# Kernel optimization log

Measured on AMD Instinct MI355X. Metric: run time of the kernel, lower is better.

Reference implementation:

```python
import jax, jax.numpy as jnp
import numpy as np

B, NQ, C = 4, 3136, 512
H_IMG, W_IMG = 56, 56
HEADS, D_MODEL, D_K, D_V = 8, 512, 512, 512
RATIO = 2
LN_EPS = 1e-3   # keras LayerNormalization default
BN_EPS = 1e-3   # keras BatchNormalization default


def setup_inputs() -> dict:
    key = jax.random.key(0)
    ks = jax.random.split(key, 16)
    s = 0.02
    inp = {
        'queries': jax.random.normal(ks[0], (B, NQ, C), jnp.float32),
        'keys': jax.random.normal(ks[1], (B, NQ, C), jnp.float32),
        'values': jax.random.normal(ks[2], (B, NQ, C), jnp.float32),
        'Wq': jax.random.normal(ks[3], (C, HEADS * D_K), jnp.float32) * s,
        'bq': jnp.zeros((HEADS * D_K,), jnp.float32),
        'Wk': jax.random.normal(ks[4], (C, HEADS * D_K), jnp.float32) * s,
        'bk': jnp.zeros((HEADS * D_K,), jnp.float32),
        'Wv': jax.random.normal(ks[5], (C, HEADS * D_V), jnp.float32) * s,
        'bv': jnp.zeros((HEADS * D_V,), jnp.float32),
        'Wo': jax.random.normal(ks[6], (HEADS * D_V, D_MODEL), jnp.float32) * s,
        'bo': jnp.zeros((D_MODEL,), jnp.float32),
        # depthwise conv: kernel (kh, kw, in_per_group=1, out=C)
        'sr_kernel': jax.random.normal(ks[7], (RATIO + 1, RATIO + 1, 1, C), jnp.float32) * s,
        'sr_bias': jnp.zeros((C,), jnp.float32),
        'ln_gamma': jnp.ones((C,), jnp.float32),
        'ln_beta': jnp.zeros((C,), jnp.float32),
        # 1x1 channels_first conv over the head axis of the score tensor
        'tw': jax.random.normal(ks[8], (HEADS, HEADS), jnp.float32) * s,
        'tb': jnp.zeros((HEADS,), jnp.float32),
        # BatchNormalization(axis=[0,1]) -> params per (batch, head)
        'bn_gamma': jnp.ones((B, HEADS), jnp.float32),
        'bn_beta': jnp.zeros((B, HEADS), jnp.float32),
    }
    return inp


def _forward(queries, keys, values, Wq, bq, Wk, bk, Wv, bv, Wo, bo,
             sr_kernel, sr_bias, ln_gamma, ln_beta, tw, tb, bn_gamma, bn_beta):
    b, nq, c = queries.shape
    # Q projection -> (b, h, nq, d_model)  (d_k == d_model)
    q = (queries @ Wq + bq).reshape(b, nq, HEADS, D_MODEL).transpose(0, 2, 1, 3)
    # spatial reduction of K/V source (ratio > 1 path; keys/values args unused)
    x = queries.reshape(b, H_IMG, W_IMG, c)
    x = jax.lax.conv_general_dilated(
        x, sr_kernel, window_strides=(RATIO, RATIO), padding='SAME',
        dimension_numbers=('NHWC', 'HWIO', 'NHWC'), feature_group_count=c) + sr_bias
    x = x.reshape(b, -1, c)  # (b, nk, c), nk = (H/ratio)*(W/ratio)
    mu = jnp.mean(x, axis=-1, keepdims=True)
    var = jnp.mean(jnp.square(x - mu), axis=-1, keepdims=True)
    x = (x - mu) * jax.lax.rsqrt(var + LN_EPS) * ln_gamma + ln_beta
    k = (x @ Wk + bk).reshape(b, -1, HEADS, D_MODEL).transpose(0, 2, 1, 3)
    v = (x @ Wv + bv).reshape(b, -1, HEADS, D_MODEL).transpose(0, 2, 1, 3)
    # scores (b, h, nq, nk)
    att = jnp.einsum('bhqd,bhkd->bhqk', q, k) / np.sqrt(D_K).astype(np.float32)
    # transform: 1x1 conv over head channel, softmax over k, BN over (q, k)
    att = jnp.einsum('bhqk,hg->bgqk', att, tw) + tb[:, None, None]
    att = jax.nn.softmax(att, axis=-1)
    m = jnp.mean(att, axis=(2, 3), keepdims=True)
    s2 = jnp.mean(jnp.square(att - m), axis=(2, 3), keepdims=True)
    att = bn_gamma[:, :, None, None] * (att - m) * jax.lax.rsqrt(s2 + BN_EPS) \
          + bn_beta[:, :, None, None]
    # attend and project out
    out = jnp.einsum('bhqk,bhkd->bhqd', att, v)
    out = out.transpose(0, 2, 1, 3).reshape(b, nq, HEADS * D_V)
    return out @ Wo + bo


def reference(queries, keys, values, Wq, bq, Wk, bk, Wv, bv, Wo, bo,
              sr_kernel, sr_bias, ln_gamma, ln_beta, tw, tb, bn_gamma, bn_beta):
    return _forward(queries, keys, values, Wq, bq, Wk, bk, Wv, bv, Wo, bo,
                    sr_kernel, sr_bias, ln_gamma, ln_beta, tw, tb, bn_gamma, bn_beta)
```

## Files before the change

### kernel.cpp

```cpp
#include <hip/hip_runtime.h>
#include <hip/hip_bf16.h>
#include <math.h>

typedef unsigned short u16;
typedef __attribute__((ext_vector_type(4))) float f32x4;
typedef __attribute__((ext_vector_type(8))) __bf16 bf16x8;

#define B_    4
#define NQ_   3136
#define C_    512
#define HIMG  56
#define WIMG  56
#define HD_   4096
#define NK_   784
#define NKP_  832

static __device__ __forceinline__ float b2f(u16 u){
  union { unsigned int i; float f; } v; v.i = ((unsigned int)u)<<16; return v.f;
}
static __device__ __forceinline__ u16 f2b(float f){
  union { float f; unsigned int i; } v; v.f = f;
  unsigned int r = v.i + 0x7fffu + ((v.i>>16)&1u);
  return (u16)(r>>16);
}

#define GLD16(gsrc, ldst) __builtin_amdgcn_global_load_lds( \
    (const __attribute__((address_space(1))) void*)(gsrc), \
    (__attribute__((address_space(3))) void*)(ldst), 16, 0, 0)

static __device__ __forceinline__ void xcd_swz(int &bx, int &by, int &bz){
  const long nx = gridDim.x, ny = gridDim.y, nz = gridDim.z;
  const long l = blockIdx.x + nx*(blockIdx.y + ny*(long)blockIdx.z);
  const long n = nx*ny*nz;
  const long q8 = n>>3, r8 = n&7;
  const long xcd = l&7, idx = l>>3;
  const long wg = (xcd<r8 ? xcd*(q8+1) : r8*(q8+1) + (xcd-r8)*q8) + idx;
  by = (int)(wg % ny);
  bx = (int)((wg/ny) % nx);
  bz = (int)(wg/(nx*ny));
}

__global__ __launch_bounds__(512)
void gemm256(const u16* __restrict__ A, const u16* __restrict__ Bm, u16* __restrict__ Cm,
             int M, int Ncols, int K, int sA, int sB, int sC, int zdiv,
             long long zA1, long long zA2, long long zB1, long long zB2,
             long long zC1, long long zC2,
             const float* __restrict__ bias1, float hscale,
             const float* __restrict__ scalePtr)
{
  __shared__ u16 lds[73728];
  int bx, by, z;
  xcd_swz(bx, by, z);
  const int zq = z / zdiv, zr = z % zdiv;
  const u16* Ab = A  + (long long)zq*zA1 + (long long)zr*zA2;
  const u16* Bb = Bm + (long long)zq*zB1 + (long long)zr*zB2;
  const int m0 = bx*256, n0 = by*128;
  const int t = threadIdx.x, w = t>>6, lane = t&63;
  const int wm = w>>1, wn = w&1;
  const int l15 = lane & 15;

  const int srow = t>>3;
  const int scol = (((t&7) ^ ((t>>3)&7)) << 3);
  const u16* aS = Ab + (long long)(m0 + srow)*sA + scol;
  const u16* bS = Bb + (long long)(n0 + srow)*sB + scol;
  const long long sA64 = (long long)64*sA, sB64 = (long long)64*sB;
  const int w512 = w*512;

#define STAGE_H0(jt, buf) do{                                     \
    const u16* a0_ = aS + (long long)(jt)*64;                     \
    u16* la_ = lds + (buf)*16384 + w512;                          \
    GLD16(a0_,            la_);                                   \
    GLD16(a0_ +   sA64,   la_ + 4096);                            \
    GLD16(a0_ + 2*sA64,   la_ + 8192);                            \
  }while(0)
#define STAGE_H1(jt, buf) do{                                     \
    const u16* a0_ = aS + (long long)(jt)*64;                     \
    const u16* b0_ = bS + (long long)(jt)*64;                     \
    u16* la_ = lds + (buf)*16384 + w512;                          \
    u16* lb_ = lds + 49152 + (buf)*8192 + w512;                   \
    GLD16(a0_ + 3*sA64,   la_ + 12288);                           \
    GLD16(b0_,            lb_);                                   \
    GLD16(b0_ +   sB64,   lb_ + 4096);                            \
  }while(0)

  f32x4 acc[4][4];
#pragma unroll
  for(int i=0;i<4;i++)
#pragma unroll
    for(int j=0;j<4;j++) acc[i][j] = (f32x4)(0.0f);

  const char* ldsc = (const char*)lds;
  const int ck0 = (((lane>>4)     ^ (lane&7)) << 4);
  const int ck1 = (((4+(lane>>4)) ^ (lane&7)) << 4);
  const int aRowB = (wm*64 + l15) * 128;
  const int bRowB = (wn*64 + l15) * 128;

  const int T = K >> 6;
  STAGE_H0(0, 0); STAGE_H1(0, 0);
  STAGE_H0(1, 1); STAGE_H1(1, 1);

  int buf = 0;
  for(int j=0; j<T; j++){
    if(j == T-1) asm volatile("s_waitcnt vmcnt(0)" ::: "memory");
    else         asm volatile("s_waitcnt vmcnt(6)" ::: "memory");
    asm volatile("s_barrier" ::: "memory");

    const int aBuf = buf*32768 + aRowB;
    const int bBuf = 98304 + buf*16384 + bRowB;
    const int nbuf = (buf+2 >= 3) ? buf-1 : buf+2;
    {
      bf16x8 af[4], bf[4];
#pragma unroll
      for(int fr=0; fr<4; fr++) af[fr] = *(const bf16x8*)(ldsc + aBuf + fr*2048 + ck0);
#pragma unroll
      for(int fn=0; fn<4; fn++) bf[fn] = *(const bf16x8*)(ldsc + bBuf + fn*2048 + ck0);
      if(j+2 < T) STAGE_H0(j+2, nbuf);
      asm volatile("s_barrier" ::: "memory");
      __builtin_amdgcn_s_setprio(1);
#pragma unroll
      for(int fr=0; fr<4; fr++)
#pragma unroll
        for(int fn=0; fn<4; fn++)
          acc[fr][fn] = __builtin_amdgcn_mfma_f32_16x16x32_bf16(af[fr], bf[fn], acc[fr][fn], 0,0,0);
      __builtin_amdgcn_s_setprio(0);
    }
    {
      bf16x8 af[4], bf[4];
#pragma unroll
      for(int fr=0; fr<4; fr++) af[fr] = *(const bf16x8*)(ldsc + aBuf + fr*2048 + ck1);
#pragma unroll
      for(int fn=0; fn<4; fn++) bf[fn] = *(const bf16x8*)(ldsc + bBuf + fn*2048 + ck1);
      if(j+2 < T) STAGE_H1(j+2, nbuf);
      asm volatile("s_barrier" ::: "memory");
      __builtin_amdgcn_s_setprio(1);
#pragma unroll
      for(int fr=0; fr<4; fr++)
#pragma unroll
        for(int fn=0; fn<4; fn++)
          acc[fr][fn] = __builtin_amdgcn_mfma_f32_16x16x32_bf16(af[fr], bf[fn], acc[fr][fn], 0,0,0);
      __builtin_amdgcn_s_setprio(0);
    }
    buf = (buf+1 >= 3) ? 0 : buf+1;
  }
#undef STAGE_H0
#undef STAGE_H1

  const float dsc = scalePtr ? scalePtr[z] : 1.0f;
  const long long cBase = (long long)zq*zC1 + (long long)zr*zC2;
  const int r4 = (lane>>4)*4;
#pragma unroll
  for(int mf=0; mf<4; mf++){
    const int row0 = m0 + wm*64 + mf*16 + r4;
#pragma unroll
    for(int nf=0; nf<4; nf++){
      const int col = n0 + wn*64 + nf*16 + l15;
      if(col < Ncols){
#pragma unroll
        for(int r=0;r<4;r++){
          const int row = row0 + r;
          if(row < M){
            float v = acc[mf][nf][r];
            if(bias1) v += bias1[col];
            Cm[cBase + (long long)row*sC + col] = f2b(v * hscale * dsc);
          }
        }
      }
    }
  }
}

template<int OUT_F32>
__global__ __launch_bounds__(256)
void gemm_bt(const u16* __restrict__ A, const u16* __restrict__ Bm, void* __restrict__ Cm,
             int M, int K, int sA, int sB, int sC, int zdiv,
             long long zA1, long long zA2, long long zB1, long long zB2,
             long long zC1, long long zC2,
             const float* __restrict__ bias1, float hscale,
             const float* __restrict__ scalePtr,
             const float* __restrict__ bias2, int rowsPerB, int b2s)
{
  __shared__ u16 lA[128*32];
  __shared__ u16 lB[128*32];
  int bx, by, z;
  xcd_swz(bx, by, z);
  const int zq = z / zdiv, zr = z % zdiv;
  const u16* Ab = A  + (long long)zq*zA1 + (long long)zr*zA2;
  const u16* Bb = Bm + (long long)zq*zB1 + (long long)zr*zB2;
  const int m0 = bx*128, n0 = by*128;
  const int t = threadIdx.x, wave = t>>6, lane = t&63;
  const int wm = (wave>>1)*64, wn = (wave&1)*64;
  const int lrow = t>>2, lcol = (t&3)*8;

  const u16* aSrc = Ab + (long long)(m0+lrow)*sA + lcol;
  const u16* bSrc = Bb + (long long)(n0+lrow)*sB + lcol;
  u16* lAw = lA + wave*512;
  u16* lBw = lB + wave*512;

  f32x4 acc[4][4];
#pragma unroll
  for(int i=0;i<4;i++)
#pragma unroll
    for(int j=0;j<4;j++) acc[i][j] = (f32x4)(0.0f);

  const int l16 = lane & 15, lk8 = (lane>>4)*8;

  for(int kk=0; kk<K; kk+=32){
    GLD16(aSrc,                    lAw);
    GLD16(aSrc + (long long)64*sA, lAw + 64*32);
    GLD16(bSrc,                    lBw);
    GLD16(bSrc + (long long)64*sB, lBw + 64*32);
    aSrc += 32; bSrc += 32;
    __syncthreads();
    bf16x8 af[4], bfr[4];
#pragma unroll
    for(int i=0;i<4;i++){
      af[i]  = *(const bf16x8*)(lA + (wm + i*16 + l16)*32 + lk8);
      bfr[i] = *(const bf16x8*)(lB + (wn + i*16 + l16)*32 + lk8);
    }
#pragma unroll
    for(int i=0;i<4;i++)
#pragma unroll
      for(int j=0;j<4;j++)
        acc[i][j] = __builtin_amdgcn_mfma_f32_16x16x32_bf16(af[i], bfr[j], acc[i][j], 0,0,0);
    __syncthreads();
  }

  const float dsc = scalePtr ? scalePtr[z] : 1.0f;
  const long long cBase = (long long)zq*zC1 + (long long)zr*zC2;
  const int rbase = (lane>>4)*4;
#pragma unroll
  for(int i=0;i<4;i++){
#pragma unroll
    for(int j=0;j<4;j++){
#pragma unroll
      for(int r=0;r<4;r++){
        const int row = m0 + wm + i*16 + rbase + r;
        const int col = n0 + wn + j*16 + l16;
        if(row < M){
          float v = acc[i][j][r];
          if(bias1) v += bias1[col];
          v *= hscale * dsc;
          if(bias2) v += bias2[(row/rowsPerB)*b2s + col];
          if(OUT_F32) ((float*)Cm)[cBase + (long long)row*sC + col] = v;
          else        ((u16*) Cm)[cBase + (long long)row*sC + col] = f2b(v);
        }
      }
    }
  }
}

__global__ __launch_bounds__(256)
void wt_kernel(const float* __restrict__ W, u16* __restrict__ Wt, int K, int N){
  __shared__ float tile[32][33];
  const int n0 = blockIdx.x*32, k0 = blockIdx.y*32;
  const int t = threadIdx.x, tr = t>>5, tc = t&31;
#pragma unroll
  for(int i=0;i<4;i++)
    tile[tr+i*8][tc] = W[(long long)(k0+tr+i*8)*N + n0+tc];
  __syncthreads();
#pragma unroll
  for(int i=0;i<4;i++)
    Wt[(long long)(n0+tr+i*8)*K + k0+tc] = f2b(tile[tc][tr+i*8]);
}

__global__ __launch_bounds__(256)
void cvt_bf16(const float* __restrict__ in, u16* __restrict__ outp, long long n){
  long long i = ((long long)blockIdx.x*256 + threadIdx.x)*4;
  if(i+3 < n){
    float4 v = *(const float4*)(in+i);
    ushort4 o; o.x=f2b(v.x); o.y=f2b(v.y); o.z=f2b(v.z); o.w=f2b(v.w);
    *(ushort4*)(outp+i) = o;
  }
}

__global__ __launch_bounds__(256)
void conv_ln(const float* __restrict__ q, const float* __restrict__ ker,
             const float* __restrict__ cbias, const float* __restrict__ gamma,
             const float* __restrict__ beta, u16* __restrict__ xo)
{
  const int p = blockIdx.x;
  const int b = p / 784, pix = p % 784;
  const int oy = pix / 28, ox = pix % 28;
  const int t = threadIdx.x;
  __shared__ float red[256];
  float v[2];
#pragma unroll
  for(int e=0;e<2;e++){
    const int c = t + e*256;
    float acc = cbias[c];
    for(int ky=0;ky<3;ky++){
      const int y = oy*2 + ky;
      if(y >= HIMG) continue;
      for(int kx=0;kx<3;kx++){
        const int x = ox*2 + kx;
        if(x >= WIMG) continue;
        acc += q[(((long long)b*HIMG + y)*WIMG + x)*C_ + c] * ker[(ky*3+kx)*C_ + c];
      }
    }
    v[e] = acc;
  }
  red[t]=v[0]+v[1]; __syncthreads();
  for(int st=128; st>0; st>>=1){ if(t<st) red[t]+=red[t+st]; __syncthreads(); }
  const float mu = red[0] * (1.0f/C_);
  __syncthreads();
  const float d0=v[0]-mu, d1=v[1]-mu;
  red[t]=d0*d0+d1*d1; __syncthreads();
  for(int st=128; st>0; st>>=1){ if(t<st) red[t]+=red[t+st]; __syncthreads(); }
  const float rs = rsqrtf(red[0]*(1.0f/C_) + 1e-3f);
  const long long ob = (long long)p*C_;
#pragma unroll
  for(int e=0;e<2;e++){
    const int c = t+e*256;
    xo[ob+c] = f2b((v[e]-mu)*rs*gamma[c] + beta[c]);
  }
}

__global__ __launch_bounds__(256)
void vt_kernel(const u16* __restrict__ Vf_b, u16* __restrict__ Vt_b, int sV){
  __shared__ u16 tile[32][33];
  const int k0 = blockIdx.x*32, d0 = blockIdx.y*32;
  const int t = threadIdx.x, tr = t>>5, tc = t&31;
#pragma unroll
  for(int i=0;i<4;i++){
    const int k = k0+tr+i*8;
    tile[tr+i*8][tc] = (k < NK_) ? Vf_b[(long long)k*sV + d0+tc] : (u16)0;
  }
  __syncthreads();
#pragma unroll
  for(int i=0;i<4;i++)
    Vt_b[(long long)(d0+tr+i*8)*NKP_ + k0+tc] = tile[tc][tr+i*8];
}

__global__ __launch_bounds__(512)
void mix_softmax(u16* __restrict__ S_b, const float* __restrict__ tw,
                 float* __restrict__ partial_b)
{
  const int qi = blockIdx.x;
  const int t = threadIdx.x;
  const int wave = t >> 6, lane = t & 63;
  __shared__ float sv[8*NK_];
  const long long rowstr = (long long)NQ_*NKP_;
  const long long base = (long long)qi*NKP_;

  for(int idx = t; idx < 8*196; idx += 512){
    const int h = idx / 196, c4 = idx % 196;
    ushort4 u4 = *(const ushort4*)(S_b + base + h*rowstr + c4*4);
    float* d = sv + h*NK_ + c4*4;
    d[0]=b2f(u4.x); d[1]=b2f(u4.y); d[2]=b2f(u4.z); d[3]=b2f(u4.w);
  }
  __syncthreads();

  const int g = wave;
  float wgt[8];
#pragma unroll
  for(int h=0;h<8;h++) wgt[h] = tw[h*8+g];

  float xs[13];
  float lmax = -1e30f;
#pragma unroll
  for(int j=0;j<13;j++){
    const int k = j*64 + lane;
    if(k < NK_){
      float x = 0.f;
#pragma unroll
      for(int h=0;h<8;h++) x += wgt[h]*sv[h*NK_+k];
      xs[j] = x;
      lmax = fmaxf(lmax, x);
    } else xs[j] = -1e30f;
  }
#pragma unroll
  for(int off=32; off>=1; off>>=1) lmax = fmaxf(lmax, __shfl_xor(lmax, off));

  float lsum = 0.f;
#pragma unroll
  for(int j=0;j<13;j++){
    const int k = j*64 + lane;
    if(k < NK_){
      const float e = __expf(xs[j] - lmax);
      xs[j] = e; lsum += e;
    }
  }
#pragma unroll
  for(int off=32; off>=1; off>>=1) lsum += __shfl_xor(lsum, off);
  const float inv = 1.0f/lsum;

  u16* dst = S_b + base + g*rowstr;
  float lss = 0.f;
#pragma unroll
  for(int j=0;j<13;j++){
    const int k = j*64 + lane;
    if(k < NK_){
      const float dev = xs[j]*inv - (1.0f/NK_);
      dst[k] = f2b(dev);
      lss += dev*dev;
    }
  }
  for(int k = NK_ + lane; k < NKP_; k += 64) dst[k] = 0;
#pragma unroll
  for(int off=32; off>=1; off>>=1) lss += __shfl_xor(lss, off);
  if(lane==0) partial_b[g*NQ_ + qi] = lss;
}

__global__ __launch_bounds__(256)
void colsum_v(const u16* __restrict__ Vf_b, float* __restrict__ cs_b, int sV){
  const int hd = blockIdx.x*256 + threadIdx.x;
  const u16* p = Vf_b + hd;
  float s=0.f;
  for(int k=0;k<NK_;k++) s += b2f(p[(long long)k*sV]);
  cs_b[hd]=s;
}

__global__ __launch_bounds__(256)
void finalize_stats(const float* __restrict__ partial_b, const float* __restrict__ bng_b,
                    const float* __restrict__ bnb_b, float* __restrict__ a_b,
                    float* __restrict__ c_b){
  const int g = blockIdx.x;
  const int t = threadIdx.x;
  __shared__ float red[4];
  float s = 0.f;
  for(int i=t; i<NQ_; i+=256) s += partial_b[g*NQ_ + i];
#pragma unroll
  for(int off=32; off>=1; off>>=1) s += __shfl_xor(s, off);
  if((t&63)==0) red[t>>6] = s;
  __syncthreads();
  if(t==0){
    const float tot = red[0]+red[1]+red[2]+red[3];
    const float s2 = tot * (1.0f/((float)NQ_*(float)NK_));
    a_b[g] = bng_b[g]*rsqrtf(s2 + 1e-3f);
    c_b[g] = bnb_b[g];
  }
}

__global__ __launch_bounds__(256)
void corr_kernel(const float* __restrict__ cs_b, const u16* __restrict__ Wot,
                 const float* __restrict__ c_b, float* __restrict__ corr_b){
  const int n = blockIdx.x, t = threadIdx.x;
  __shared__ float red[256];
  float s = 0.f;
  for(int hd=t; hd<HD_; hd+=256)
    s += c_b[hd>>9] * cs_b[hd] * b2f(Wot[(long long)n*HD_+hd]);
  red[t]=s; __syncthreads();
  for(int st=128; st>0; st>>=1){ if(t<st) red[t]+=red[t+st]; __syncthreads(); }
  if(t==0) corr_b[n]=red[0];
}

extern "C" void kernel_launch(void* const* d_in, const int* in_sizes, int n_in,
                              void* d_out, int out_size, void* d_ws, size_t ws_size,
                              hipStream_t stream)
{
  (void)in_sizes; (void)n_in; (void)out_size;
  const float* queries = (const float*)d_in[0];
  const float* Wq  = (const float*)d_in[3];
  const float* bq  = (const float*)d_in[4];
  const float* Wk  = (const float*)d_in[5];
  const float* bk  = (const float*)d_in[6];
  const float* Wv  = (const float*)d_in[7];
  const float* bv  = (const float*)d_in[8];
  const float* Wo  = (const float*)d_in[9];
  const float* bo  = (const float*)d_in[10];
  const float* srk = (const float*)d_in[11];
  const float* srb = (const float*)d_in[12];
  const float* lng = (const float*)d_in[13];
  const float* lnb = (const float*)d_in[14];
  const float* tw  = (const float*)d_in[15];
  const float* bng = (const float*)d_in[17];
  const float* bnb = (const float*)d_in[18];
  float* out = (float*)d_out;
  const float QSC = 0.04419417382415922f;

  char* w = (char*)d_ws;
  size_t off = 0;
  auto alloc = [&](size_t bytes)->char*{
    char* p = w + off; off += (bytes + 255) & ~(size_t)255; return p;
  };

  const bool tierA = (ws_size >= (size_t)210*1024*1024);

  u16* Wqt = (u16*)alloc((size_t)HD_*C_*2);
  u16* Wkt = (u16*)alloc((size_t)HD_*C_*2);
  u16* Wvt = (u16*)alloc((size_t)HD_*C_*2);
  u16* Wot = (u16*)alloc((size_t)C_*HD_*2);
  u16* x   = (u16*)alloc((size_t)B_*NK_*C_*2 + 262144);
  float* bkv = (float*)alloc((size_t)2*HD_*4);
  u16* Qin;
  u16* QfU;
  if(tierA){
    Qin = (u16*)alloc((size_t)B_*NQ_*C_*2);
    QfU = (u16*)alloc((size_t)B_*NQ_*HD_*2);
  } else {
    Qin = (u16*)alloc((size_t)NQ_*C_*2 + 262144);
    QfU = (u16*)alloc((size_t)NQ_*HD_*2);
  }
  u16* KV_b = (u16*)alloc((size_t)NK_*2*HD_*2 + 4194304);
  u16* Vt_b = (u16*)alloc((size_t)HD_*NKP_*2);
  u16* S_b  = (u16*)alloc((size_t)8*NQ_*NKP_*2 + 524288);
  float* colsum  = (float*)alloc((size_t)B_*HD_*4);
  float* partial = (float*)alloc((size_t)8*NQ_*4);
  float* aArr    = (float*)alloc(256);
  float* cArr    = (float*)alloc(256);
  float* corrB   = (float*)alloc((size_t)B_*C_*4);

  wt_kernel<<<dim3(128,16), 256, 0, stream>>>(Wq, Wqt, 512, 4096);
  wt_kernel<<<dim3(128,16), 256, 0, stream>>>(Wk, Wkt, 512, 4096);
  wt_kernel<<<dim3(128,16), 256, 0, stream>>>(Wv, Wvt, 512, 4096);
  wt_kernel<<<dim3(16,128), 256, 0, stream>>>(Wo, Wot, 4096, 512);
  conv_ln<<<B_*NK_, 256, 0, stream>>>(queries, srk, srb, lng, lnb, x);
  hipMemcpyAsync(bkv,      bk, HD_*4, hipMemcpyDeviceToDevice, stream);
  hipMemcpyAsync(bkv+HD_,  bv, HD_*4, hipMemcpyDeviceToDevice, stream);

  if(tierA){
    cvt_bf16<<<6272, 256, 0, stream>>>(queries, Qin, (long long)B_*NQ_*C_);
    gemm256<<<dim3(49,32,1),512,0,stream>>>(Qin, Wqt, QfU, B_*NQ_, 4096, 512,
        512, 512, HD_, 1, 0,0,0,0,0,0, bq, QSC, nullptr);
  }

  for(int b=0; b<B_; b++){
    u16* Qf_b = tierA ? (QfU + (size_t)b*NQ_*HD_) : QfU;
    if(!tierA){
      cvt_bf16<<<1568, 256, 0, stream>>>(queries + (size_t)b*NQ_*C_, Qin, (long long)NQ_*C_);
      gemm256<<<dim3(13,32,1),512,0,stream>>>(Qin, Wqt, Qf_b, NQ_, 4096, 512,
          512, 512, HD_, 1, 0,0,0,0,0,0, bq, QSC, nullptr);
    }
    const u16* x_b = x + (size_t)b*NK_*C_;
    gemm256<<<dim3(4,64,1),512,0,stream>>>(x_b, Wkt, KV_b, NK_, 2*HD_, 512,
        512, 512, 2*HD_, 1, 0,0,0,0,0,0, bkv, 1.0f, nullptr);
    vt_kernel<<<dim3(26,128),256,0,stream>>>(KV_b + HD_, Vt_b, 2*HD_);
    colsum_v<<<16,256,0,stream>>>(KV_b + HD_, colsum + b*HD_, 2*HD_);
    gemm256<<<dim3(13,7,8),512,0,stream>>>(Qf_b, KV_b, S_b, NQ_, NKP_, 512,
        HD_, 2*HD_, NKP_, 8, 0, 512, 0, 512, 0, (long long)NQ_*NKP_,
        nullptr, 1.0f, nullptr);
    mix_softmax<<<NQ_, 512, 0, stream>>>(S_b, tw, partial);
    finalize_stats<<<8,256,0,stream>>>(partial, bng + b*8, bnb + b*8, aArr + b*8, cArr + b*8);
    corr_kernel<<<512,256,0,stream>>>(colsum + b*HD_, Wot, cArr + b*8, corrB + b*C_);
    gemm256<<<dim3(13,4,8),512,0,stream>>>(S_b, Vt_b, Qf_b, NQ_, 512, NKP_,
        NKP_, NKP_, HD_, 8, 0, (long long)NQ_*NKP_, 0, (long long)512*NKP_, 0, 512,
        nullptr, 1.0f, aArr + b*8);
    if(!tierA){
      gemm_bt<1><<<dim3(25,4,1),256,0,stream>>>(Qf_b, Wot, out + (size_t)b*NQ_*C_,
          NQ_, HD_, HD_, HD_, C_,
          1, 0,0,0,0,0,0, bo, 1.0f, nullptr, corrB + b*C_, NQ_, C_);
    }
  }

  if(tierA){
    gemm_bt<1><<<dim3(98,4,1),256,0,stream>>>(QfU, Wot, out, B_*NQ_, HD_, HD_, HD_, C_,
        1, 0,0,0,0,0,0, bo, 1.0f, nullptr, corrB, NQ_, C_);
  }
}
```

Measured before the change: 1.013 ms.

## Replace 256x128 and simple GEMMs with unified double-buffered 128x128 kernel

Removes the 512-thread 256x128 triple-buffered GEMM and the simple single-buffered gemm_bt. Both are replaced by one templated 128x128-tile, 256-thread kernel with K-step 64, XOR-swizzled LDS, and a double buffer filled by async global-to-LDS loads. All GEMM launches, including the output projection, now use this kernel with grids adjusted for the smaller tiles. This gives more blocks and lower LDS use per block, and a pipelined output projection. In exchange, each block reuses less data per tile and the prefetch pipeline is shallower than the old triple buffer.

```diff
diff --git a/kernel.cpp b/kernel.cpp
--- a/kernel.cpp
+++ b/kernel.cpp
@@ -40,161 +40,48 @@
   bz = (int)(wg/(nx*ny));
 }
 
-__global__ __launch_bounds__(512)
-void gemm256(const u16* __restrict__ A, const u16* __restrict__ Bm, u16* __restrict__ Cm,
+template<int OUT_F32>
+__global__ __launch_bounds__(256)
+void gemm128(const u16* __restrict__ A, const u16* __restrict__ Bm, void* __restrict__ Cm,
              int M, int Ncols, int K, int sA, int sB, int sC, int zdiv,
-             long long zA1, long long zA2, long long zB1, long long zB2,
-             long long zC1, long long zC2,
-             const float* __restrict__ bias1, float hscale,
-             const float* __restrict__ scalePtr)
-{
-  __shared__ u16 lds[73728];
-  int bx, by, z;
-  xcd_swz(bx, by, z);
-  const int zq = z / zdiv, zr = z % zdiv;
-  const u16* Ab = A  + (long long)zq*zA1 + (long long)zr*zA2;
-  const u16* Bb = Bm + (long long)zq*zB1 + (long long)zr*zB2;
-  const int m0 = bx*256, n0 = by*128;
-  const int t = threadIdx.x, w = t>>6, lane = t&63;
-  const int wm = w>>1, wn = w&1;
-  const int l15 = lane & 15;
-
-  const int srow = t>>3;
-  const int scol = (((t&7) ^ ((t>>3)&7)) << 3);
-  const u16* aS = Ab + (long long)(m0 + srow)*sA + scol;
-  const u16* bS = Bb + (long long)(n0 + srow)*sB + scol;
-  const long long sA64 = (long long)64*sA, sB64 = (long long)64*sB;
-  const int w512 = w*512;
-
-#define STAGE_H0(jt, buf) do{                                     \
-    const u16* a0_ = aS + (long long)(jt)*64;                     \
-    u16* la_ = lds + (buf)*16384 + w512;                          \
-    GLD16(a0_,            la_);                                   \
-    GLD16(a0_ +   sA64,   la_ + 4096);                            \
-    GLD16(a0_ + 2*sA64,   la_ + 8192);                            \
-  }while(0)
-#define STAGE_H1(jt, buf) do{                                     \
-    const u16* a0_ = aS + (long long)(jt)*64;                     \
-    const u16* b0_ = bS + (long long)(jt)*64;                     \
-    u16* la_ = lds + (buf)*16384 + w512;                          \
-    u16* lb_ = lds + 49152 + (buf)*8192 + w512;                   \
-    GLD16(a0_ + 3*sA64,   la_ + 12288);                           \
-    GLD16(b0_,            lb_);                                   \
-    GLD16(b0_ +   sB64,   lb_ + 4096);                            \
-  }while(0)
-
-  f32x4 acc[4][4];
-#pragma unroll
-  for(int i=0;i<4;i++)
-#pragma unroll
-    for(int j=0;j<4;j++) acc[i][j] = (f32x4)(0.0f);
-
-  const char* ldsc = (const char*)lds;
-  const int ck0 = (((lane>>4)     ^ (lane&7)) << 4);
-  const int ck1 = (((4+(lane>>4)) ^ (lane&7)) << 4);
-  const int aRowB = (wm*64 + l15) * 128;
-  const int bRowB = (wn*64 + l15) * 128;
-
-  const int T = K >> 6;
-  STAGE_H0(0, 0); STAGE_H1(0, 0);
-  STAGE_H0(1, 1); STAGE_H1(1, 1);
-
-  int buf = 0;
-  for(int j=0; j<T; j++){
-    if(j == T-1) asm volatile("s_waitcnt vmcnt(0)" ::: "memory");
-    else         asm volatile("s_waitcnt vmcnt(6)" ::: "memory");
-    asm volatile("s_barrier" ::: "memory");
-
-    const int aBuf = buf*32768 + aRowB;
-    const int bBuf = 98304 + buf*16384 + bRowB;
-    const int nbuf = (buf+2 >= 3) ? buf-1 : buf+2;
-    {
-      bf16x8 af[4], bf[4];
-#pragma unroll
-      for(int fr=0; fr<4; fr++) af[fr] = *(const bf16x8*)(ldsc + aBuf + fr*2048 + ck0);
-#pragma unroll
-      for(int fn=0; fn<4; fn++) bf[fn] = *(const bf16x8*)(ldsc + bBuf + fn*2048 + ck0);
-      if(j+2 < T) STAGE_H0(j+2, nbuf);
-      asm volatile("s_barrier" ::: "memory");
-      __builtin_amdgcn_s_setprio(1);
-#pragma unroll
-      for(int fr=0; fr<4; fr++)
-#pragma unroll
-        for(int fn=0; fn<4; fn++)
-          acc[fr][fn] = __builtin_amdgcn_mfma_f32_16x16x32_bf16(af[fr], bf[fn], acc[fr][fn], 0,0,0);
-      __builtin_amdgcn_s_setprio(0);
-    }
-    {
-      bf16x8 af[4], bf[4];
-#pragma unroll
-      for(int fr=0; fr<4; fr++) af[fr] = *(const bf16x8*)(ldsc + aBuf + fr*2048 + ck1);
-#pragma unroll
-      for(int fn=0; fn<4; fn++) bf[fn] = *(const bf16x8*)(ldsc + bBuf + fn*2048 + ck1);
-      if(j+2 < T) STAGE_H1(j+2, nbuf);
-      asm volatile("s_barrier" ::: "memory");
-      __builtin_amdgcn_s_setprio(1);
-#pragma unroll
-      for(int fr=0; fr<4; fr++)
-#pragma unroll
-        for(int fn=0; fn<4; fn++)
-          acc[fr][fn] = __builtin_amdgcn_mfma_f32_16x16x32_bf16(af[fr], bf[fn], acc[fr][fn], 0,0,0);
-      __builtin_amdgcn_s_setprio(0);
-    }
-    buf = (buf+1 >= 3) ? 0 : buf+1;
-  }
-#undef STAGE_H0
-#undef STAGE_H1
-
-  const float dsc = scalePtr ? scalePtr[z] : 1.0f;
-  const long long cBase = (long long)zq*zC1 + (long long)zr*zC2;
-  const int r4 = (lane>>4)*4;
-#pragma unroll
-  for(int mf=0; mf<4; mf++){
-    const int row0 = m0 + wm*64 + mf*16 + r4;
-#pragma unroll
-    for(int nf=0; nf<4; nf++){
-      const int col = n0 + wn*64 + nf*16 + l15;
-      if(col < Ncols){
-#pragma unroll
-        for(int r=0;r<4;r++){
-          const int row = row0 + r;
-          if(row < M){
-            float v = acc[mf][nf][r];
-            if(bias1) v += bias1[col];
-            Cm[cBase + (long long)row*sC + col] = f2b(v * hscale * dsc);
-          }
-        }
-      }
-    }
-  }
-}
-
-template<int OUT_F32>
-__global__ __launch_bounds__(256)
-void gemm_bt(const u16* __restrict__ A, const u16* __restrict__ Bm, void* __restrict__ Cm,
-             int M, int K, int sA, int sB, int sC, int zdiv,
              long long zA1, long long zA2, long long zB1, long long zB2,
              long long zC1, long long zC2,
              const float* __restrict__ bias1, float hscale,
              const float* __restrict__ scalePtr,
              const float* __restrict__ bias2, int rowsPerB, int b2s)
 {
-  __shared__ u16 lA[128*32];
-  __shared__ u16 lB[128*32];
+  __shared__ u16 lds[32768];
   int bx, by, z;
   xcd_swz(bx, by, z);
   const int zq = z / zdiv, zr = z % zdiv;
   const u16* Ab = A  + (long long)zq*zA1 + (long long)zr*zA2;
   const u16* Bb = Bm + (long long)zq*zB1 + (long long)zr*zB2;
   const int m0 = bx*128, n0 = by*128;
-  const int t = threadIdx.x, wave = t>>6, lane = t&63;
-  const int wm = (wave>>1)*64, wn = (wave&1)*64;
-  const int lrow = t>>2, lcol = (t&3)*8;
-
-  const u16* aSrc = Ab + (long long)(m0+lrow)*sA + lcol;
-  const u16* bSrc = Bb + (long long)(n0+lrow)*sB + lcol;
-  u16* lAw = lA + wave*512;
-  u16* lBw = lB + wave*512;
+  const int t = threadIdx.x, w = t>>6, lane = t&63;
+  const int wm = w>>1, wn = w&1;
+  const int l15 = lane & 15;
+
+  const int srow = t>>3;
+  const int scol = (((t&7) ^ (srow&7)) << 3);
+  const u16* aS = Ab + (long long)(m0 + srow)*sA + scol;
+  const u16* bS = Bb + (long long)(n0 + srow)*sB + scol;
+  const long long sA32 = (long long)32*sA, sB32 = (long long)32*sB;
+  const int w512 = w*512;
+
+#define STAGE(jt, buf) do{                                        \
+    const u16* a0_ = aS + (long long)(jt)*64;                     \
+    const u16* b0_ = bS + (long long)(jt)*64;                     \
+    u16* la_ = lds + (buf)*8192 + w512;                           \
+    u16* lb_ = lds + 16384 + (buf)*8192 + w512;                   \
+    GLD16(a0_,            la_);                                   \
+    GLD16(a0_ +   sA32,   la_ + 2048);                            \
+    GLD16(a0_ + 2*sA32,   la_ + 4096);                            \
+    GLD16(a0_ + 3*sA32,   la_ + 6144);                            \
+    GLD16(b0_,            lb_);                                   \
+    GLD16(b0_ +   sB32,   lb_ + 2048);                            \
+    GLD16(b0_ + 2*sB32,   lb_ + 4096);                            \
+    GLD16(b0_ + 3*sB32,   lb_ + 6144);                            \
+  }while(0)
 
   f32x4 acc[4][4];
 #pragma unroll
@@ -202,47 +89,78 @@
 #pragma unroll
     for(int j=0;j<4;j++) acc[i][j] = (f32x4)(0.0f);
 
-  const int l16 = lane & 15, lk8 = (lane>>4)*8;
-
-  for(int kk=0; kk<K; kk+=32){
-    GLD16(aSrc,                    lAw);
-    GLD16(aSrc + (long long)64*sA, lAw + 64*32);
-    GLD16(bSrc,                    lBw);
-    GLD16(bSrc + (long long)64*sB, lBw + 64*32);
-    aSrc += 32; bSrc += 32;
-    __syncthreads();
-    bf16x8 af[4], bfr[4];
-#pragma unroll
-    for(int i=0;i<4;i++){
-      af[i]  = *(const bf16x8*)(lA + (wm + i*16 + l16)*32 + lk8);
-      bfr[i] = *(const bf16x8*)(lB + (wn + i*16 + l16)*32 + lk8);
-    }
-#pragma unroll
-    for(int i=0;i<4;i++)
-#pragma unroll
-      for(int j=0;j<4;j++)
-        acc[i][j] = __builtin_amdgcn_mfma_f32_16x16x32_bf16(af[i], bfr[j], acc[i][j], 0,0,0);
-    __syncthreads();
-  }
+  const char* ldsc = (const char*)lds;
+  const int ck0 = (((lane>>4)     ^ (lane&7)) << 4);
+  const int ck1 = (((4+(lane>>4)) ^ (lane&7)) << 4);
+  const int aRowB = (wm*64 + l15) * 128;
+  const int bRowB = (wn*64 + l15) * 128;
+
+  const int T = K >> 6;
+  STAGE(0, 0);
+  STAGE(1, 1);
+
+  for(int j=0; j<T; j++){
+    const int bj = j & 1;
+    if(j == T-1) asm volatile("s_waitcnt vmcnt(0)" ::: "memory");
+    else         asm volatile("s_waitcnt vmcnt(8)" ::: "memory");
+    asm volatile("s_barrier" ::: "memory");
+
+    const int aBuf = bj*16384 + aRowB;
+    const int bBuf = 32768 + bj*16384 + bRowB;
+    {
+      bf16x8 af[4], bf[4];
+#pragma unroll
+      for(int fr=0; fr<4; fr++) af[fr] = *(const bf16x8*)(ldsc + aBuf + fr*2048 + ck0);
+#pragma unroll
+      for(int fn=0; fn<4; fn++) bf[fn] = *(const bf16x8*)(ldsc + bBuf + fn*2048 + ck0);
+      __builtin_amdgcn_s_setprio(1);
+#pragma unroll
+      for(int fr=0; fr<4; fr++)
+#pragma unroll
+        for(int fn=0; fn<4; fn++)
+          acc[fr][fn] = __builtin_amdgcn_mfma_f32_16x16x32_bf16(af[fr], bf[fn], acc[fr][fn], 0,0,0);
+      __builtin_amdgcn_s_setprio(0);
+    }
+    {
+      bf16x8 af[4], bf[4];
+#pragma unroll
+      for(int fr=0; fr<4; fr++) af[fr] = *(const bf16x8*)(ldsc + aBuf + fr*2048 + ck1);
+#pragma unroll
+      for(int fn=0; fn<4; fn++) bf[fn] = *(const bf16x8*)(ldsc + bBuf + fn*2048 + ck1);
+      __builtin_amdgcn_s_setprio(1);
+#pragma unroll
+      for(int fr=0; fr<4; fr++)
+#pragma unroll
+        for(int fn=0; fn<4; fn++)
+          acc[fr][fn] = __builtin_amdgcn_mfma_f32_16x16x32_bf16(af[fr], bf[fn], acc[fr][fn], 0,0,0);
+      __builtin_amdgcn_s_setprio(0);
+    }
+    asm volatile("s_barrier" ::: "memory");
+    if(j+2 < T) STAGE(j+2, bj);
+  }
+#undef STAGE
 
   const float dsc = scalePtr ? scalePtr[z] : 1.0f;
   const long long cBase = (long long)zq*zC1 + (long long)zr*zC2;
-  const int rbase = (lane>>4)*4;
-#pragma unroll
-  for(int i=0;i<4;i++){
-#pragma unroll
-    for(int j=0;j<4;j++){
-#pragma unroll
-      for(int r=0;r<4;r++){
-        const int row = m0 + wm + i*16 + rbase + r;
-        const int col = n0 + wn + j*16 + l16;
-        if(row < M){
-          float v = acc[i][j][r];
-          if(bias1) v += bias1[col];
-          v *= hscale * dsc;
-          if(bias2) v += bias2[(row/rowsPerB)*b2s + col];
-          if(OUT_F32) ((float*)Cm)[cBase + (long long)row*sC + col] = v;
-          else        ((u16*) Cm)[cBase + (long long)row*sC + col] = f2b(v);
+  const int r4 = (lane>>4)*4;
+#pragma unroll
+  for(int mf=0; mf<4; mf++){
+    const int row0 = m0 + wm*64 + mf*16 + r4;
+#pragma unroll
+    for(int nf=0; nf<4; nf++){
+      const int col = n0 + wn*64 + nf*16 + l15;
+      if(col < Ncols){
+#pragma unroll
+        for(int r=0;r<4;r++){
+          const int row = row0 + r;
+          if(row < M){
+            float v = acc[mf][nf][r];
+            if(bias1) v += bias1[col];
+            v *= hscale * dsc;
+            if(bias2) v += bias2[(row/rowsPerB)*b2s + col];
+            if(OUT_F32) ((float*)Cm)[cBase + (long long)row*sC + col] = v;
+            else        ((u16*) Cm)[cBase + (long long)row*sC + col] = f2b(v);
+          }
         }
       }
     }
@@ -510,40 +428,40 @@
 
   if(tierA){
     cvt_bf16<<<6272, 256, 0, stream>>>(queries, Qin, (long long)B_*NQ_*C_);
-    gemm256<<<dim3(49,32,1),512,0,stream>>>(Qin, Wqt, QfU, B_*NQ_, 4096, 512,
-        512, 512, HD_, 1, 0,0,0,0,0,0, bq, QSC, nullptr);
+    gemm128<0><<<dim3(98,32,1),256,0,stream>>>(Qin, Wqt, QfU, B_*NQ_, 4096, 512,
+        512, 512, HD_, 1, 0,0,0,0,0,0, bq, QSC, nullptr, nullptr, 1, 0);
   }
 
   for(int b=0; b<B_; b++){
     u16* Qf_b = tierA ? (QfU + (size_t)b*NQ_*HD_) : QfU;
     if(!tierA){
       cvt_bf16<<<1568, 256, 0, stream>>>(queries + (size_t)b*NQ_*C_, Qin, (long long)NQ_*C_);
-      gemm256<<<dim3(13,32,1),512,0,stream>>>(Qin, Wqt, Qf_b, NQ_, 4096, 512,
-          512, 512, HD_, 1, 0,0,0,0,0,0, bq, QSC, nullptr);
+      gemm128<0><<<dim3(25,32,1),256,0,stream>>>(Qin, Wqt, Qf_b, NQ_, 4096, 512,
+          512, 512, HD_, 1, 0,0,0,0,0,0, bq, QSC, nullptr, nullptr, 1, 0);
     }
     const u16* x_b = x + (size_t)b*NK_*C_;
-    gemm256<<<dim3(4,64,1),512,0,stream>>>(x_b, Wkt, KV_b, NK_, 2*HD_, 512,
-        512, 512, 2*HD_, 1, 0,0,0,0,0,0, bkv, 1.0f, nullptr);
+    gemm128<0><<<dim3(7,64,1),256,0,stream>>>(x_b, Wkt, KV_b, NK_, 2*HD_, 512,
+        512, 512, 2*HD_, 1, 0,0,0,0,0,0, bkv, 1.0f, nullptr, nullptr, 1, 0);
     vt_kernel<<<dim3(26,128),256,0,stream>>>(KV_b + HD_, Vt_b, 2*HD_);
     colsum_v<<<16,256,0,stream>>>(KV_b + HD_, colsum + b*HD_, 2*HD_);
-    gemm256<<<dim3(13,7,8),512,0,stream>>>(Qf_b, KV_b, S_b, NQ_, NKP_, 512,
+    gemm128<0><<<dim3(25,7,8),256,0,stream>>>(Qf_b, KV_b, S_b, NQ_, NKP_, 512,
         HD_, 2*HD_, NKP_, 8, 0, 512, 0, 512, 0, (long long)NQ_*NKP_,
-        nullptr, 1.0f, nullptr);
+        nullptr, 1.0f, nullptr, nullptr, 1, 0);
     mix_softmax<<<NQ_, 512, 0, stream>>>(S_b, tw, partial);
     finalize_stats<<<8,256,0,stream>>>(partial, bng + b*8, bnb + b*8, aArr + b*8, cArr + b*8);
     corr_kernel<<<512,256,0,stream>>>(colsum + b*HD_, Wot, cArr + b*8, corrB + b*C_);
-    gemm256<<<dim3(13,4,8),512,0,stream>>>(S_b, Vt_b, Qf_b, NQ_, 512, NKP_,
+    gemm128<0><<<dim3(25,4,8),256,0,stream>>>(S_b, Vt_b, Qf_b, NQ_, 512, NKP_,
         NKP_, NKP_, HD_, 8, 0, (long long)NQ_*NKP_, 0, (long long)512*NKP_, 0, 512,
-        nullptr, 1.0f, aArr + b*8);
+        nullptr, 1.0f, aArr + b*8, nullptr, 1, 0);
     if(!tierA){
-      gemm_bt<1><<<dim3(25,4,1),256,0,stream>>>(Qf_b, Wot, out + (size_t)b*NQ_*C_,
-          NQ_, HD_, HD_, HD_, C_,
+      gemm128<1><<<dim3(25,4,1),256,0,stream>>>(Qf_b, Wot, out + (size_t)b*NQ_*C_,
+          NQ_, 512, HD_, HD_, HD_, C_,
           1, 0,0,0,0,0,0, bo, 1.0f, nullptr, corrB + b*C_, NQ_, C_);
     }
   }
 
   if(tierA){
-    gemm_bt<1><<<dim3(98,4,1),256,0,stream>>>(QfU, Wot, out, B_*NQ_, HD_, HD_, HD_, C_,
-        1, 0,0,0,0,0,0, bo, 1.0f, nullptr, corrB, NQ_, C_);
-  }
-}
+    gemm128<1><<<dim3(98,4,1),256,0,stream>>>(QfU, Wot, out, B_*NQ_, 512, HD_,
+        HD_, HD_, C_, 1, 0,0,0,0,0,0, bo, 1.0f, nullptr, corrB, NQ_, C_);
+  }
+}
```

After: 1.008 ms. About the same (-0.5%).
